# Kernel tuning notes

Measured on AMD Instinct MI355X. Metric: run time of the kernel, lower is better.

## Reference

```python
import jax, jax.numpy as jnp
import numpy as np

B, N, C = 2, 50000, 81          # images, proposals/image, classes (incl. background)
H, W = 800.0, 1333.0            # image shape
SCORE_THRESH = 0.05
NMS_THRESH = 0.5
DETS = 100                      # detections_per_img
K = 2048                        # pre-NMS candidates kept per image (padded)
BBOX_CLIP = 4.135166556742356   # log(1000/16), torchvision BoxCoder clamp
WX, WY, WW, WH = 10.0, 10.0, 5.0, 5.0  # bbox_reg_weights
MIN_SIZE = 0.01                 # remove_small_boxes threshold
LBL_OFFSET = 1401.0             # MAX_SIZE + 1, batched_nms class-offset trick


def setup_inputs() -> dict:
    key = jax.random.key(0)
    k1, k2, k3, k4 = jax.random.split(key, 4)
    class_logits = jax.random.normal(k1, (B * N, C), jnp.float32) * 2.0
    box_regression = jax.random.normal(k2, (B * N, C * 4), jnp.float32) * 0.5
    wh_img = jnp.array([W, H], jnp.float32)
    cxy = jax.random.uniform(k3, (B, N, 2), jnp.float32) * wh_img
    wh = jax.random.uniform(k4, (B, N, 2), jnp.float32) * 200.0 + 4.0
    x1y1 = jnp.clip(cxy - 0.5 * wh, 0.0, wh_img)
    x2y2 = jnp.clip(cxy + 0.5 * wh, 0.0, wh_img)
    proposals = jnp.concatenate([x1y1, x2y2], axis=-1)  # [B, N, 4] xyxy
    return {"class_logits": class_logits, "box_regression": box_regression, "proposals": proposals}


def _decode(rel, boxes):
    # rel [N, C, 4], boxes [N, 4] xyxy -> decoded [N, C, 4] (torchvision BoxCoder.decode)
    w = boxes[:, 2] - boxes[:, 0]
    h = boxes[:, 3] - boxes[:, 1]
    cx = boxes[:, 0] + 0.5 * w
    cy = boxes[:, 1] + 0.5 * h
    dx = rel[..., 0] / WX
    dy = rel[..., 1] / WY
    dw = jnp.minimum(rel[..., 2] / WW, BBOX_CLIP)
    dh = jnp.minimum(rel[..., 3] / WH, BBOX_CLIP)
    pcx = dx * w[:, None] + cx[:, None]
    pcy = dy * h[:, None] + cy[:, None]
    pw = jnp.exp(dw) * w[:, None]
    ph = jnp.exp(dh) * h[:, None]
    return jnp.stack([pcx - 0.5 * pw, pcy - 0.5 * ph, pcx + 0.5 * pw, pcy + 0.5 * ph], axis=-1)


def _pairwise_iou(a):
    # a [K, 4] -> [K, K]
    area = (a[:, 2] - a[:, 0]) * (a[:, 3] - a[:, 1])
    lt = jnp.maximum(a[:, None, :2], a[None, :, :2])
    rb = jnp.minimum(a[:, None, 2:], a[None, :, 2:])
    wh = jnp.clip(rb - lt, 0.0)
    inter = wh[..., 0] * wh[..., 1]
    return inter / (area[:, None] + area[None, :] - inter + 1e-9)


def _nms_keep(iou, valid):
    # sequential greedy NMS over score-sorted candidates
    Kn = iou.shape[0]
    def body(keep, i):
        sup = jnp.any(keep & (iou[i] > NMS_THRESH))
        keep = keep.at[i].set(valid[i] & ~sup)
        return keep, None
    keep, _ = jax.lax.scan(body, jnp.zeros((Kn,), bool), jnp.arange(Kn))
    return keep


def _per_image(logits, reg, props):
    # logits [N, C], reg [N, C*4], props [N, 4]
    scores = jax.nn.softmax(logits, axis=-1)[:, 1:]                  # drop background
    boxes = _decode(reg.reshape(N, C, 4), props)[:, 1:]              # [N, C-1, 4]
    boxes = jnp.stack([jnp.clip(boxes[..., 0], 0.0, W),
                       jnp.clip(boxes[..., 1], 0.0, H),
                       jnp.clip(boxes[..., 2], 0.0, W),
                       jnp.clip(boxes[..., 3], 0.0, H)], axis=-1)
    fb = boxes.reshape(-1, 4)                                        # [N*(C-1), 4]
    fs = scores.reshape(-1)
    fl = jnp.broadcast_to(jnp.arange(1, C), (N, C - 1)).reshape(-1)
    ws = fb[:, 2] - fb[:, 0]
    hs = fb[:, 3] - fb[:, 1]
    valid = (fs > SCORE_THRESH) & (ws >= MIN_SIZE) & (hs >= MIN_SIZE)
    masked = jnp.where(valid, fs, -1.0)
    top_s, top_i = jax.lax.top_k(masked, K)                          # sorted desc
    cb = fb[top_i]
    cl = fl[top_i]
    cvalid = top_s > 0.0
    # batched NMS: offset boxes by class so different classes never overlap
    ob = cb + cl.astype(cb.dtype)[:, None] * LBL_OFFSET
    keep = _nms_keep(_pairwise_iou(ob), cvalid)
    kept_s = jnp.where(keep, top_s, -1.0)
    out_s, sel = jax.lax.top_k(kept_s, DETS)
    m = out_s > 0.0
    out_b = cb[sel] * m[:, None].astype(cb.dtype)
    out_l = jnp.where(m, cl[sel], -1)
    return out_b, jnp.where(m, out_s, 0.0), out_l


def reference(class_logits, box_regression, proposals):
    logits = class_logits.reshape(B, N, C)
    reg = box_regression.reshape(B, N, C * 4)
    boxes, scores, labels = jax.vmap(_per_image)(logits, reg, proposals)
    return boxes, scores, labels  # [B, DETS, 4], [B, DETS], [B, DETS] (padded, score==0 invalid)
```

## Files before the change

kernel.cpp:

```cpp
#include <hip/hip_runtime.h>
#include <hip/hip_bf16.h>
#include <stdint.h>

#define Bn 2
#define Np 50000
#define Cc 81
#define CM1 80
#define KSEL 2048
#define NDET 100
#define NBUCK 2048
#define BUCK_BASE 0x3D000000u
#define BUCK_SHIFT 15
#define SELCAP 4096
#define IMG_W 1333.0f
#define IMG_H 800.0f
#define SCORE_TH 0.05f
#define MIN_SZ 0.01f
#define NMS_TH 0.5f
#define LBLOFF 1401.0f
#define BBOX_CLIP_F 4.135166556742356f
#define CHUNK 16
#define QCAP 320
#define BLKX 782
#define WPI  (BLKX*4)
#define RS_WPB 4

typedef unsigned long long u64;
typedef unsigned int u32;

__device__ __forceinline__ u64 shfl64(u64 v, int src) {
  int lo = __shfl((int)(u32)v, src, 64);
  int hi = __shfl((int)(u32)(v >> 32), src, 64);
  return ((u64)(u32)hi << 32) | (u32)lo;
}

__device__ __forceinline__ void decode_box(int row, int c,
    const float* __restrict__ reg, const float* __restrict__ props,
    float& x1, float& y1, float& x2, float& y2) {
  const float4 pr = *reinterpret_cast<const float4*>(props + (size_t)row * 4);
  float w = __fsub_rn(pr.z, pr.x), h = __fsub_rn(pr.w, pr.y);
  float cx = __fadd_rn(pr.x, 0.5f * w), cy = __fadd_rn(pr.y, 0.5f * h);
  const float4 rel = *reinterpret_cast<const float4*>(reg + ((size_t)row * Cc + c) * 4);
  float dx = __fdiv_rn(rel.x, 10.f), dy = __fdiv_rn(rel.y, 10.f);
  float dw = fminf(__fdiv_rn(rel.z, 5.f), BBOX_CLIP_F);
  float dh = fminf(__fdiv_rn(rel.w, 5.f), BBOX_CLIP_F);
  float pcx = __fadd_rn(__fmul_rn(dx, w), cx);
  float pcy = __fadd_rn(__fmul_rn(dy, h), cy);
  float pw = __fmul_rn(expf(dw), w);
  float ph = __fmul_rn(expf(dh), h);
  x1 = fminf(fmaxf(__fsub_rn(pcx, 0.5f * pw), 0.f), IMG_W);
  y1 = fminf(fmaxf(__fsub_rn(pcy, 0.5f * ph), 0.f), IMG_H);
  x2 = fminf(fmaxf(__fadd_rn(pcx, 0.5f * pw), 0.f), IMG_W);
  y2 = fminf(fmaxf(__fadd_rn(pcy, 0.5f * ph), 0.f), IMG_H);
}

#define SOFTMAX_PROLOG(S)                                            \
  const int p = lane >> 2, qd = lane & 3;                            \
  const int base = p * Cc + qd * 21;                                 \
  const int cnt_k = (qd == 3) ? 18 : 21;                             \
  float ev[21];                                                      \
  _Pragma("unroll")                                                  \
  for (int k = 0; k < 21; ++k)                                       \
    ev[k] = (k < cnt_k) ? (S)[base + k] : -3.4e38f;                  \
  float m = ev[0];                                                   \
  _Pragma("unroll")                                                  \
  for (int k = 1; k < 21; ++k) m = fmaxf(m, ev[k]);                  \
  m = fmaxf(m, __shfl_xor(m, 1, 64));                                \
  m = fmaxf(m, __shfl_xor(m, 2, 64));                                \
  float s = 0.f;                                                     \
  _Pragma("unroll")                                                  \
  for (int k = 0; k < 21; ++k) {                                     \
    ev[k] = (k < cnt_k) ? expf(ev[k] - m) : 0.f;                     \
    s += ev[k];                                                      \
  }                                                                  \
  s += __shfl_xor(s, 1, 64);                                         \
  s += __shfl_xor(s, 2, 64);                                         \
  const float thr = SCORE_TH * s;

#define STAGE_LOGITS(S, src)                                         \
  _Pragma("unroll")                                                  \
  for (int i = 0; i < 6; ++i) {                                      \
    const int f4 = i * 64 + lane;                                    \
    if (f4 < (CHUNK * Cc) / 4) {                                     \
      const float4 v = *reinterpret_cast<const float4*>((src) + (size_t)f4 * 4); \
      *reinterpret_cast<float4*>(&(S)[f4 * 4]) = v;                  \
    }                                                                \
  }

__global__ __launch_bounds__(256, 4) void passA_kernel(
    const float* __restrict__ logits, const float* __restrict__ reg,
    const float* __restrict__ props, u64* __restrict__ wseg,
    u32* __restrict__ wcnt, u32* __restrict__ ghist)
{
  __shared__ __align__(16) float stg[4][CHUNK * Cc];
  __shared__ u64 qbuf[4][QCAP];
  __shared__ u32 hist[NBUCK];
  const int b = blockIdx.y;
  const int tid = threadIdx.x;
  const int wave = tid >> 6, lane = tid & 63;
  for (int i = tid; i < NBUCK; i += 256) hist[i] = 0;
  __syncthreads();

  const int wslot = (blockIdx.x << 2) + wave;
  const int n0 = wslot * CHUNK;
  u64* Q = qbuf[wave];
  u32 qcnt = 0;
  if (n0 < Np) {
    float* S = stg[wave];
    STAGE_LOGITS(S, logits + ((size_t)b * Np + n0) * Cc)
    SOFTMAX_PROLOG(S)
    const int n_ = n0 + p;
    #pragma unroll
    for (int k = 0; k < 21; ++k) {
      const int c = qd * 21 + k;
      bool emit = false;
      u64 key = 0;
      if (c > 0 && ev[k] > thr) {
        const u32 sb = __float_as_uint(__fdiv_rn(ev[k], s));
        const u32 idx = (u32)(n_ * CM1 + (c - 1));
        key = ((u64)sb << 32) | (u32)(~idx);
        emit = true;
      }
      const u64 bal = __ballot(emit);
      if (emit) Q[qcnt + (u32)__popcll(bal & ((1ull << lane) - 1ull))] = key;
      qcnt += (u32)__popcll(bal);
    }
  }
  u64* seg = wseg + (size_t)(b * WPI + wslot) * QCAP;
  u32 wout = 0;
  for (u32 qb = 0; qb < qcnt; qb += 64) {
    const bool act = (qb + (u32)lane) < qcnt;
    u64 key = act ? Q[qb + lane] : 0ull;
    bool valid = false;
    u32 sb = 0;
    if (act) {
      sb = (u32)(key >> 32);
      const u32 idx = ~(u32)key;
      const int pn = (int)(idx / CM1);
      const int c = (int)(idx - (u32)pn * CM1) + 1;
      float x1, y1, x2, y2;
      decode_box(b * Np + pn, c, reg, props, x1, y1, x2, y2);
      valid = (__fsub_rn(x2, x1) >= MIN_SZ) && (__fsub_rn(y2, y1) >= MIN_SZ);
    }
    const u64 bal = __ballot(valid);
    if (valid) {
      const u32 pos = wout + (u32)__popcll(bal & ((1ull << lane) - 1ull));
      seg[pos] = key;
      u32 bk = (sb - BUCK_BASE) >> BUCK_SHIFT;
      if (bk > (u32)(NBUCK - 1)) bk = NBUCK - 1;
      atomicAdd(&hist[bk], 1u);
    }
    wout += (u32)__popcll(bal);
  }
  if (lane == 0) wcnt[b * WPI + wslot] = wout;
  __syncthreads();
  for (int i = tid; i < NBUCK; i += 256) {
    const u32 v = hist[i];
    if (v) atomicAdd(&ghist[b * NBUCK + i], v);
  }
}

__global__ void thresh_kernel(const u32* __restrict__ ghist, u32* __restrict__ gT,
                              u32* __restrict__ gTot, u32* __restrict__ boffs) {
  const int b = blockIdx.x;
  const int lane = threadIdx.x;
  const u32* h = ghist + b * NBUCK;
  u32* bo = boffs + b * NBUCK;
  const int SEG = NBUCK / 64;
  u32 segsum = 0;
  for (int t = 0; t < SEG; ++t) segsum += h[lane * SEG + t];
  u32 suf = segsum;
  #pragma unroll
  for (int o = 1; o < 64; o <<= 1) {
    const u32 v = (u32)__shfl_down((int)suf, o, 64);
    if (lane + o < 64) suf += v;
  }
  u32 acc = suf - segsum;
  int myT = -1; u32 totv = 0;
  for (int t = SEG - 1; t >= 0; --t) {
    const int bk = lane * SEG + t;
    bo[bk] = acc;
    acc += h[bk];
    if (myT < 0 && acc >= (u32)KSEL) { myT = bk; totv = acc; }
  }
  int Tg = myT;
  #pragma unroll
  for (int o = 32; o; o >>= 1) Tg = max(Tg, __shfl_xor(Tg, o, 64));
  if (Tg < 0) {
    if (lane == 0) { gT[b] = 0u; gTot[b] = (acc < (u32)SELCAP) ? acc : (u32)SELCAP; }
  } else if (myT == Tg) {
    gT[b] = (u32)Tg;
    gTot[b] = (totv < (u32)SELCAP) ? totv : (u32)SELCAP;
  }
}

__global__ __launch_bounds__(256) void scatter_kernel(
    const u64* __restrict__ wseg, const u32* __restrict__ wcnt,
    const u32* __restrict__ gT, const u32* __restrict__ boffs,
    u32* __restrict__ bfill, u64* __restrict__ skeys)
{
  const int b = blockIdx.y;
  const u32 T = gT[b];
  const int wave = threadIdx.x >> 6, lane = threadIdx.x & 63;
  const u32 sgi = blockIdx.x * 4 + wave;
  if (sgi >= (u32)WPI) return;
  const u32 cnt = wcnt[b * WPI + sgi];
  const u64* seg = wseg + (size_t)(b * WPI + sgi) * QCAP;
  for (u32 i = lane; i < cnt; i += 64) {
    const u64 key = seg[i];
    const u32 sb = (u32)(key >> 32);
    u32 bk = (sb - BUCK_BASE) >> BUCK_SHIFT;
    if (bk > (u32)(NBUCK - 1)) bk = NBUCK - 1;
    if (bk >= T) {
      const u32 pos = boffs[b * NBUCK + bk] + atomicAdd(&bfill[b * NBUCK + bk], 1u);
      if (pos < (u32)SELCAP) skeys[(size_t)b * SELCAP + pos] = key;
    }
  }
}

__global__ __launch_bounds__(256) void runsort_kernel(
    const u64* __restrict__ skeys, u64* __restrict__ skeys2,
    const u32* __restrict__ gT, const u32* __restrict__ gTot,
    const u32* __restrict__ boffs, const u32* __restrict__ bfill)
{
  const int b = blockIdx.y;
  const int wave = threadIdx.x >> 6, lane = threadIdx.x & 63;
  const u32 bk = blockIdx.x * RS_WPB + wave;
  if (bk >= (u32)NBUCK || bk < gT[b]) return;
  const u32 total = gTot[b];
  const u32 start = boffs[b * NBUCK + bk];
  u32 L = bfill[b * NBUCK + bk];
  if (L == 0 || start >= (u32)KSEL || start >= total) return;
  if (start + L > total) L = total - start;
  const u64* run = skeys + (size_t)b * SELCAP + start;
  u64* dst = skeys2 + (size_t)b * SELCAP + start;
  if (L <= 128u) {
    const u64 k0 = (lane < (int)L) ? run[lane] : 0ull;
    const u64 k1 = (64 + lane < (int)L) ? run[64 + lane] : 0ull;
    u32 r0 = 0, r1 = 0;
    #pragma unroll
    for (int l = 0; l < 64; ++l) {
      const u64 o0 = shfl64(k0, l);
      const u64 o1 = shfl64(k1, l);
      r0 += (o0 > k0) + (o1 > k0);
      r1 += (o0 > k1) + (o1 > k1);
    }
    if (lane < (int)L) dst[r0] = k0;
    if (64 + lane < (int)L) dst[r1] = k1;
  } else {
    for (u32 i = lane; i < L; i += 64) {
      const u64 k = run[i];
      u32 r = 0;
      for (u32 q = 0; q < L; ++q) r += (run[q] > k);
      dst[r] = k;
    }
  }
}

__global__ __launch_bounds__(1024) void tail_kernel(
    const u64* __restrict__ skeys2, const u32* __restrict__ gTot,
    const float* __restrict__ reg, const float* __restrict__ props,
    float* __restrict__ out)
{
  __shared__ u64 keys[KSEL];
  __shared__ float obx1[KSEL], oby1[KSEL], obx2[KSEL], oby2[KSEL];
  __shared__ float oar[KSEL], osc[KSEL];
  __shared__ unsigned short keptIdx[NDET];
  __shared__ u32 supflags[64];
  __shared__ u32 sh_kc;
  const int b = blockIdx.x;
  const int tid = threadIdx.x;
  const int wave = tid >> 6, lane = tid & 63;
  const u32 total = gTot[b];
  if (tid == 0) sh_kc = 0;

  for (int i = tid; i < KSEL; i += 1024)
    keys[i] = (i < (int)total) ? skeys2[(size_t)b * SELCAP + i] : 0ull;
  __syncthreads();

  for (int t = tid; t < KSEL; t += 1024) {
    const u64 key = keys[t];
    float x1 = 0, y1 = 0, x2 = 0, y2 = 0, score = 0, lab = 0;
    if (key) {
      const u32 sb = (u32)(key >> 32);
      const u32 idx = ~(u32)key;
      const int n_ = (int)(idx / CM1);
      const int c = (int)(idx % CM1) + 1;
      score = __uint_as_float(sb);
      decode_box(b * Np + n_, c, reg, props, x1, y1, x2, y2);
      lab = (float)c;
    }
    const float offv = __fmul_rn(lab, LBLOFF);
    const float ox1 = __fadd_rn(x1, offv), oy1 = __fadd_rn(y1, offv);
    const float ox2 = __fadd_rn(x2, offv), oy2 = __fadd_rn(y2, offv);
    obx1[t] = ox1; oby1[t] = oy1; obx2[t] = ox2; oby2[t] = oy2;
    oar[t] = __fmul_rn(__fsub_rn(ox2, ox1), __fsub_rn(oy2, oy1));
    osc[t] = score;
  }
  __syncthreads();

  int kc = 0;
  for (int c = 0; c < 32 && kc < NDET; ++c) {
    if (tid < 64) supflags[tid] = 0;
    __syncthreads();
    const int j = (c << 6) + lane;
    const float cx1 = obx1[j], cy1 = oby1[j], cx2 = obx2[j], cy2 = oby2[j], ca = oar[j];
    bool sup = false;
    for (int k = wave; k < kc; k += 16) {
      const int ki = keptIdx[k];
      const float ltx = fmaxf(cx1, obx1[ki]), lty = fmaxf(cy1, oby1[ki]);
      const float rbx = fminf(cx2, obx2[ki]), rby = fminf(cy2, oby2[ki]);
      const float wx = fmaxf(__fsub_rn(rbx, ltx), 0.f);
      const float wy = fmaxf(__fsub_rn(rby, lty), 0.f);
      const float inter = __fmul_rn(wx, wy);
      const float denom = __fadd_rn(__fsub_rn(__fadd_rn(ca, oar[ki]), inter), 1e-9f);
      if (__fdiv_rn(inter, denom) > NMS_TH) sup = true;
    }
    if (sup) supflags[lane] = 1u;
    __syncthreads();
    if (wave == 0) {
      u64 rem = __ballot(supflags[lane] != 0u);
      u64 todo = __ballot(osc[j] > 0.f) & ~rem;
      int kcl = kc;
      while (todo && kcl < NDET) {
        const int jb = (int)__builtin_ctzll(todo);
        const int cj = (c << 6) + jb;
        if (lane == 0) keptIdx[kcl] = (unsigned short)cj;
        ++kcl;
        const float kx1 = obx1[cj], ky1 = oby1[cj], kx2 = obx2[cj], ky2 = oby2[cj], ka = oar[cj];
        const float ltx = fmaxf(kx1, cx1), lty = fmaxf(ky1, cy1);
        const float rbx = fminf(kx2, cx2), rby = fminf(ky2, cy2);
        const float wx = fmaxf(__fsub_rn(rbx, ltx), 0.f);
        const float wy = fmaxf(__fsub_rn(rby, lty), 0.f);
        const float inter = __fmul_rn(wx, wy);
        const float denom = __fadd_rn(__fsub_rn(__fadd_rn(ka, ca), inter), 1e-9f);
        const u64 w = __ballot(__fdiv_rn(inter, denom) > NMS_TH);
        rem |= w;
        todo &= ~rem;
        todo &= ~(1ull << jb);
      }
      if (lane == 0) sh_kc = (u32)kcl;
    }
    __syncthreads();
    kc = (int)sh_kc;
  }

  __syncthreads();
  const int kcl = (kc < NDET) ? kc : NDET;
  if (tid < NDET) {
    float bx1 = 0, by1 = 0, bx2 = 0, by2 = 0, sc = 0, lb = -1.f;
    if (tid < kcl) {
      const int i = keptIdx[tid];
      const u64 key = keys[i];
      const u32 idx = ~(u32)key;
      const int n_ = (int)(idx / CM1);
      const int cc = (int)(idx % CM1) + 1;
      decode_box(b * Np + n_, cc, reg, props, bx1, by1, bx2, by2);
      sc = osc[i];
      lb = (float)cc;
    }
    float* ob = out + (size_t)b * NDET * 4;
    ob[tid * 4 + 0] = bx1; ob[tid * 4 + 1] = by1;
    ob[tid * 4 + 2] = bx2; ob[tid * 4 + 3] = by2;
    out[Bn * NDET * 4 + b * NDET + tid] = sc;
    out[Bn * NDET * 4 + Bn * NDET + b * NDET + tid] = lb;
  }
}

extern "C" void kernel_launch(void* const* d_in, const int* in_sizes, int n_in,
                              void* d_out, int out_size, void* d_ws, size_t ws_size,
                              hipStream_t stream) {
  const float* logits = (const float*)d_in[0];
  const float* reg    = (const float*)d_in[1];
  const float* props  = (const float*)d_in[2];
  float* out = (float*)d_out;
  char* ws = (char*)d_ws;

  u32* gT   = (u32*)ws;
  u32* gTot = (u32*)(ws + 16);
  size_t off = 64;
  u32* ghist  = (u32*)(ws + off); off += (size_t)Bn * NBUCK * 4;
  u32* bfill  = (u32*)(ws + off); off += (size_t)Bn * NBUCK * 4;
  const size_t memset_bytes = off;
  u32* boffs  = (u32*)(ws + off); off += (size_t)Bn * NBUCK * 4;
  u64* skeys  = (u64*)(ws + off); off += (size_t)Bn * SELCAP * 8;
  u64* skeys2 = (u64*)(ws + off); off += (size_t)Bn * SELCAP * 8;
  u32* wcnt   = (u32*)(ws + off); off += (size_t)Bn * WPI * 4;
  off = (off + 255) & ~(size_t)255;
  u64* wseg   = (u64*)(ws + off); off += (size_t)Bn * WPI * QCAP * 8;
  (void)ws_size;

  hipMemsetAsync(d_ws, 0, memset_bytes, stream);
  passA_kernel<<<dim3(BLKX, Bn), 256, 0, stream>>>(logits, reg, props, wseg, wcnt, ghist);
  thresh_kernel<<<dim3(Bn), 64, 0, stream>>>(ghist, gT, gTot, boffs);
  scatter_kernel<<<dim3((WPI + 3) / 4, Bn), 256, 0, stream>>>(wseg, wcnt, gT, boffs, bfill, skeys);
  runsort_kernel<<<dim3(NBUCK / RS_WPB, Bn), 256, 0, stream>>>(skeys, skeys2, gT, gTot, boffs, bfill);
  tail_kernel<<<dim3(Bn), 1024, 0, stream>>>(skeys2, gTot, reg, props, out);
}
```

Baseline: 85.50 us.

## Defer box decode and size filter to scatter; single-wave streaming NMS tail

Pass A no longer decodes boxes for every above-threshold candidate. The histogram now counts keys before the min-size filter, and the decode plus size check run only for keys in buckets at or above the threshold inside the scatter kernel. The run-sort kernel decodes the sorted keys into a structure-of-arrays selection buffer and zero-fills slots left by filtered boxes. The tail kernel becomes one 64-thread wave that walks the candidates in 64-wide chunks and exits early once 100 boxes are kept, instead of a 1024-thread block that decodes all 2048 candidates and synchronises each step. The risks are that the bucket threshold now counts invalid boxes, and that the serial tail may lengthen when many candidates are suppressed.

```diff
diff --git a/kernel.cpp b/kernel.cpp
--- a/kernel.cpp
+++ b/kernel.cpp
@@ -54,6 +54,21 @@
   y2 = fminf(fmaxf(__fadd_rn(pcy, 0.5f * ph), 0.f), IMG_H);
 }
 
+__device__ __forceinline__ void decode_key_to_sel(u64 key, int b,
+    const float* __restrict__ reg, const float* __restrict__ props,
+    float* __restrict__ S, u32 pos) {
+  const u32 sb = (u32)(key >> 32);
+  const u32 idx = ~(u32)key;
+  const int n_ = (int)(idx / CM1);
+  const int c = (int)(idx % CM1) + 1;
+  float x1, y1, x2, y2;
+  decode_box(b * Np + n_, c, reg, props, x1, y1, x2, y2);
+  S[0 * SELCAP + pos] = x1; S[1 * SELCAP + pos] = y1;
+  S[2 * SELCAP + pos] = x2; S[3 * SELCAP + pos] = y2;
+  S[4 * SELCAP + pos] = __uint_as_float(sb);
+  S[5 * SELCAP + pos] = (float)c;
+}
+
 #define SOFTMAX_PROLOG(S)                                            \
   const int p = lane >> 2, qd = lane & 3;                            \
   const int base = p * Cc + qd * 21;                                 \
@@ -88,12 +103,10 @@
   }
 
 __global__ __launch_bounds__(256, 4) void passA_kernel(
-    const float* __restrict__ logits, const float* __restrict__ reg,
-    const float* __restrict__ props, u64* __restrict__ wseg,
+    const float* __restrict__ logits, u64* __restrict__ wseg,
     u32* __restrict__ wcnt, u32* __restrict__ ghist)
 {
   __shared__ __align__(16) float stg[4][CHUNK * Cc];
-  __shared__ u64 qbuf[4][QCAP];
   __shared__ u32 hist[NBUCK];
   const int b = blockIdx.y;
   const int tid = threadIdx.x;
@@ -103,8 +116,8 @@
 
   const int wslot = (blockIdx.x << 2) + wave;
   const int n0 = wslot * CHUNK;
-  u64* Q = qbuf[wave];
-  u32 qcnt = 0;
+  u64* seg = wseg + (size_t)(b * WPI + wslot) * QCAP;
+  u32 wout = 0;
   if (n0 < Np) {
     float* S = stg[wave];
     STAGE_LOGITS(S, logits + ((size_t)b * Np + n0) * Cc)
@@ -114,43 +127,22 @@
     for (int k = 0; k < 21; ++k) {
       const int c = qd * 21 + k;
       bool emit = false;
-      u64 key = 0;
+      u64 key = 0; u32 bk = 0;
       if (c > 0 && ev[k] > thr) {
         const u32 sb = __float_as_uint(__fdiv_rn(ev[k], s));
         const u32 idx = (u32)(n_ * CM1 + (c - 1));
         key = ((u64)sb << 32) | (u32)(~idx);
+        bk = (sb - BUCK_BASE) >> BUCK_SHIFT;
+        if (bk > (u32)(NBUCK - 1)) bk = NBUCK - 1;
         emit = true;
       }
       const u64 bal = __ballot(emit);
-      if (emit) Q[qcnt + (u32)__popcll(bal & ((1ull << lane) - 1ull))] = key;
-      qcnt += (u32)__popcll(bal);
-    }
-  }
-  u64* seg = wseg + (size_t)(b * WPI + wslot) * QCAP;
-  u32 wout = 0;
-  for (u32 qb = 0; qb < qcnt; qb += 64) {
-    const bool act = (qb + (u32)lane) < qcnt;
-    u64 key = act ? Q[qb + lane] : 0ull;
-    bool valid = false;
-    u32 sb = 0;
-    if (act) {
-      sb = (u32)(key >> 32);
-      const u32 idx = ~(u32)key;
-      const int pn = (int)(idx / CM1);
-      const int c = (int)(idx - (u32)pn * CM1) + 1;
-      float x1, y1, x2, y2;
-      decode_box(b * Np + pn, c, reg, props, x1, y1, x2, y2);
-      valid = (__fsub_rn(x2, x1) >= MIN_SZ) && (__fsub_rn(y2, y1) >= MIN_SZ);
-    }
-    const u64 bal = __ballot(valid);
-    if (valid) {
-      const u32 pos = wout + (u32)__popcll(bal & ((1ull << lane) - 1ull));
-      seg[pos] = key;
-      u32 bk = (sb - BUCK_BASE) >> BUCK_SHIFT;
-      if (bk > (u32)(NBUCK - 1)) bk = NBUCK - 1;
-      atomicAdd(&hist[bk], 1u);
-    }
-    wout += (u32)__popcll(bal);
+      if (emit) {
+        seg[wout + (u32)__popcll(bal & ((1ull << lane) - 1ull))] = key;
+        atomicAdd(&hist[bk], 1u);
+      }
+      wout += (u32)__popcll(bal);
+    }
   }
   if (lane == 0) wcnt[b * WPI + wslot] = wout;
   __syncthreads();
@@ -197,7 +189,8 @@
 __global__ __launch_bounds__(256) void scatter_kernel(
     const u64* __restrict__ wseg, const u32* __restrict__ wcnt,
     const u32* __restrict__ gT, const u32* __restrict__ boffs,
-    u32* __restrict__ bfill, u64* __restrict__ skeys)
+    u32* __restrict__ bfill, u64* __restrict__ skeys,
+    const float* __restrict__ reg, const float* __restrict__ props)
 {
   const int b = blockIdx.y;
   const u32 T = gT[b];
@@ -212,31 +205,43 @@
     u32 bk = (sb - BUCK_BASE) >> BUCK_SHIFT;
     if (bk > (u32)(NBUCK - 1)) bk = NBUCK - 1;
     if (bk >= T) {
-      const u32 pos = boffs[b * NBUCK + bk] + atomicAdd(&bfill[b * NBUCK + bk], 1u);
-      if (pos < (u32)SELCAP) skeys[(size_t)b * SELCAP + pos] = key;
+      const u32 idx = ~(u32)key;
+      const int pn = (int)(idx / CM1);
+      const int c = (int)(idx % CM1) + 1;
+      float x1, y1, x2, y2;
+      decode_box(b * Np + pn, c, reg, props, x1, y1, x2, y2);
+      if (__fsub_rn(x2, x1) >= MIN_SZ && __fsub_rn(y2, y1) >= MIN_SZ) {
+        const u32 pos = boffs[b * NBUCK + bk] + atomicAdd(&bfill[b * NBUCK + bk], 1u);
+        if (pos < (u32)SELCAP) skeys[(size_t)b * SELCAP + pos] = key;
+      }
     }
   }
 }
 
 __global__ __launch_bounds__(256) void runsort_kernel(
-    const u64* __restrict__ skeys, u64* __restrict__ skeys2,
-    const u32* __restrict__ gT, const u32* __restrict__ gTot,
-    const u32* __restrict__ boffs, const u32* __restrict__ bfill)
+    const u64* __restrict__ skeys, const u32* __restrict__ gT,
+    const u32* __restrict__ boffs, const u32* __restrict__ bfill,
+    const u32* __restrict__ ghist,
+    const float* __restrict__ reg, const float* __restrict__ props,
+    float* __restrict__ sel)
 {
   const int b = blockIdx.y;
   const int wave = threadIdx.x >> 6, lane = threadIdx.x & 63;
   const u32 bk = blockIdx.x * RS_WPB + wave;
   if (bk >= (u32)NBUCK || bk < gT[b]) return;
-  const u32 total = gTot[b];
   const u32 start = boffs[b * NBUCK + bk];
-  u32 L = bfill[b * NBUCK + bk];
-  if (L == 0 || start >= (u32)KSEL || start >= total) return;
-  if (start + L > total) L = total - start;
+  if (start >= (u32)SELCAP) return;
+  u32 Lp = bfill[b * NBUCK + bk];
+  u32 Lh = ghist[b * NBUCK + bk];
+  if (start + Lp > (u32)SELCAP) Lp = SELCAP - start;
+  if (start + Lh > (u32)SELCAP) Lh = SELCAP - start;
+  float* S = sel + (size_t)b * 6 * SELCAP;
+  for (u32 j = Lp + lane; j < Lh; j += 64) S[4 * SELCAP + start + j] = 0.f;
+  if (Lp == 0) return;
   const u64* run = skeys + (size_t)b * SELCAP + start;
-  u64* dst = skeys2 + (size_t)b * SELCAP + start;
-  if (L <= 128u) {
-    const u64 k0 = (lane < (int)L) ? run[lane] : 0ull;
-    const u64 k1 = (64 + lane < (int)L) ? run[64 + lane] : 0ull;
+  if (Lp <= 128u) {
+    const u64 k0 = (lane < (int)Lp) ? run[lane] : 0ull;
+    const u64 k1 = (64 + lane < (int)Lp) ? run[64 + lane] : 0ull;
     u32 r0 = 0, r1 = 0;
     #pragma unroll
     for (int l = 0; l < 64; ++l) {
@@ -245,125 +250,89 @@
       r0 += (o0 > k0) + (o1 > k0);
       r1 += (o0 > k1) + (o1 > k1);
     }
-    if (lane < (int)L) dst[r0] = k0;
-    if (64 + lane < (int)L) dst[r1] = k1;
+    if (lane < (int)Lp) decode_key_to_sel(k0, b, reg, props, S, start + r0);
+    if (64 + lane < (int)Lp) decode_key_to_sel(k1, b, reg, props, S, start + r1);
   } else {
-    for (u32 i = lane; i < L; i += 64) {
+    for (u32 i = lane; i < Lp; i += 64) {
       const u64 k = run[i];
       u32 r = 0;
-      for (u32 q = 0; q < L; ++q) r += (run[q] > k);
-      dst[r] = k;
-    }
-  }
-}
-
-__global__ __launch_bounds__(1024) void tail_kernel(
-    const u64* __restrict__ skeys2, const u32* __restrict__ gTot,
-    const float* __restrict__ reg, const float* __restrict__ props,
+      for (u32 q = 0; q < Lp; ++q) r += (run[q] > k);
+      decode_key_to_sel(k, b, reg, props, S, start + r);
+    }
+  }
+}
+
+__global__ __launch_bounds__(64) void tail_kernel(
+    const float* __restrict__ sel, const u32* __restrict__ gTot,
     float* __restrict__ out)
 {
-  __shared__ u64 keys[KSEL];
-  __shared__ float obx1[KSEL], oby1[KSEL], obx2[KSEL], oby2[KSEL];
-  __shared__ float oar[KSEL], osc[KSEL];
-  __shared__ unsigned short keptIdx[NDET];
-  __shared__ u32 supflags[64];
-  __shared__ u32 sh_kc;
+  __shared__ float kox1[NDET], koy1[NDET], kox2[NDET], koy2[NDET], kar[NDET];
+  __shared__ float kx1[NDET], ky1[NDET], kx2[NDET], ky2[NDET], ksc[NDET], klb[NDET];
   const int b = blockIdx.x;
-  const int tid = threadIdx.x;
-  const int wave = tid >> 6, lane = tid & 63;
+  const int lane = threadIdx.x;
   const u32 total = gTot[b];
-  if (tid == 0) sh_kc = 0;
-
-  for (int i = tid; i < KSEL; i += 1024)
-    keys[i] = (i < (int)total) ? skeys2[(size_t)b * SELCAP + i] : 0ull;
-  __syncthreads();
-
-  for (int t = tid; t < KSEL; t += 1024) {
-    const u64 key = keys[t];
-    float x1 = 0, y1 = 0, x2 = 0, y2 = 0, score = 0, lab = 0;
-    if (key) {
-      const u32 sb = (u32)(key >> 32);
-      const u32 idx = ~(u32)key;
-      const int n_ = (int)(idx / CM1);
-      const int c = (int)(idx % CM1) + 1;
-      score = __uint_as_float(sb);
-      decode_box(b * Np + n_, c, reg, props, x1, y1, x2, y2);
-      lab = (float)c;
-    }
-    const float offv = __fmul_rn(lab, LBLOFF);
+  const float* S = sel + (size_t)b * 6 * SELCAP;
+  int kc = 0;
+  for (u32 bbase = 0; bbase < total && kc < NDET; bbase += 64) {
+    const u32 pos = bbase + lane;
+    const bool inb = pos < total;
+    float x1 = 0, y1 = 0, x2 = 0, y2 = 0, sc = 0, lb = 0;
+    if (inb) {
+      x1 = S[0 * SELCAP + pos]; y1 = S[1 * SELCAP + pos];
+      x2 = S[2 * SELCAP + pos]; y2 = S[3 * SELCAP + pos];
+      sc = S[4 * SELCAP + pos]; lb = S[5 * SELCAP + pos];
+    }
+    const float offv = __fmul_rn(lb, LBLOFF);
     const float ox1 = __fadd_rn(x1, offv), oy1 = __fadd_rn(y1, offv);
     const float ox2 = __fadd_rn(x2, offv), oy2 = __fadd_rn(y2, offv);
-    obx1[t] = ox1; oby1[t] = oy1; obx2[t] = ox2; oby2[t] = oy2;
-    oar[t] = __fmul_rn(__fsub_rn(ox2, ox1), __fsub_rn(oy2, oy1));
-    osc[t] = score;
-  }
-  __syncthreads();
-
-  int kc = 0;
-  for (int c = 0; c < 32 && kc < NDET; ++c) {
-    if (tid < 64) supflags[tid] = 0;
-    __syncthreads();
-    const int j = (c << 6) + lane;
-    const float cx1 = obx1[j], cy1 = oby1[j], cx2 = obx2[j], cy2 = oby2[j], ca = oar[j];
+    const float ar = __fmul_rn(__fsub_rn(ox2, ox1), __fsub_rn(oy2, oy1));
+    const bool valid = inb && (sc > 0.f);
     bool sup = false;
-    for (int k = wave; k < kc; k += 16) {
-      const int ki = keptIdx[k];
-      const float ltx = fmaxf(cx1, obx1[ki]), lty = fmaxf(cy1, oby1[ki]);
-      const float rbx = fminf(cx2, obx2[ki]), rby = fminf(cy2, oby2[ki]);
+    for (int k = 0; k < kc; ++k) {
+      const float ltx = fmaxf(ox1, kox1[k]), lty = fmaxf(oy1, koy1[k]);
+      const float rbx = fminf(ox2, kox2[k]), rby = fminf(oy2, koy2[k]);
       const float wx = fmaxf(__fsub_rn(rbx, ltx), 0.f);
       const float wy = fmaxf(__fsub_rn(rby, lty), 0.f);
       const float inter = __fmul_rn(wx, wy);
-      const float denom = __fadd_rn(__fsub_rn(__fadd_rn(ca, oar[ki]), inter), 1e-9f);
+      const float denom = __fadd_rn(__fsub_rn(__fadd_rn(ar, kar[k]), inter), 1e-9f);
       if (__fdiv_rn(inter, denom) > NMS_TH) sup = true;
     }
-    if (sup) supflags[lane] = 1u;
-    __syncthreads();
-    if (wave == 0) {
-      u64 rem = __ballot(supflags[lane] != 0u);
-      u64 todo = __ballot(osc[j] > 0.f) & ~rem;
-      int kcl = kc;
-      while (todo && kcl < NDET) {
-        const int jb = (int)__builtin_ctzll(todo);
-        const int cj = (c << 6) + jb;
-        if (lane == 0) keptIdx[kcl] = (unsigned short)cj;
-        ++kcl;
-        const float kx1 = obx1[cj], ky1 = oby1[cj], kx2 = obx2[cj], ky2 = oby2[cj], ka = oar[cj];
-        const float ltx = fmaxf(kx1, cx1), lty = fmaxf(ky1, cy1);
-        const float rbx = fminf(kx2, cx2), rby = fminf(ky2, cy2);
-        const float wx = fmaxf(__fsub_rn(rbx, ltx), 0.f);
-        const float wy = fmaxf(__fsub_rn(rby, lty), 0.f);
-        const float inter = __fmul_rn(wx, wy);
-        const float denom = __fadd_rn(__fsub_rn(__fadd_rn(ka, ca), inter), 1e-9f);
-        const u64 w = __ballot(__fdiv_rn(inter, denom) > NMS_TH);
-        rem |= w;
-        todo &= ~rem;
-        todo &= ~(1ull << jb);
+    u64 rem = __ballot(sup) | ~__ballot(valid);
+    u64 todo = ~rem;
+    while (todo && kc < NDET) {
+      const int jb = (int)__builtin_ctzll(todo);
+      const float bx1 = __shfl(ox1, jb, 64), by1 = __shfl(oy1, jb, 64);
+      const float bx2 = __shfl(ox2, jb, 64), by2 = __shfl(oy2, jb, 64);
+      const float ba  = __shfl(ar, jb, 64);
+      if (lane == jb) {
+        kox1[kc] = ox1; koy1[kc] = oy1; kox2[kc] = ox2; koy2[kc] = oy2; kar[kc] = ar;
+        kx1[kc] = x1; ky1[kc] = y1; kx2[kc] = x2; ky2[kc] = y2; ksc[kc] = sc; klb[kc] = lb;
       }
-      if (lane == 0) sh_kc = (u32)kcl;
-    }
-    __syncthreads();
-    kc = (int)sh_kc;
-  }
-
-  __syncthreads();
+      const float ltx = fmaxf(ox1, bx1), lty = fmaxf(oy1, by1);
+      const float rbx = fminf(ox2, bx2), rby = fminf(oy2, by2);
+      const float wx = fmaxf(__fsub_rn(rbx, ltx), 0.f);
+      const float wy = fmaxf(__fsub_rn(rby, lty), 0.f);
+      const float inter = __fmul_rn(wx, wy);
+      const float denom = __fadd_rn(__fsub_rn(__fadd_rn(ar, ba), inter), 1e-9f);
+      const u64 w = __ballot(__fdiv_rn(inter, denom) > NMS_TH);
+      rem |= w;
+      todo &= ~rem;
+      todo &= ~(1ull << jb);
+      ++kc;
+    }
+  }
   const int kcl = (kc < NDET) ? kc : NDET;
-  if (tid < NDET) {
+  for (int k = lane; k < NDET; k += 64) {
     float bx1 = 0, by1 = 0, bx2 = 0, by2 = 0, sc = 0, lb = -1.f;
-    if (tid < kcl) {
-      const int i = keptIdx[tid];
-      const u64 key = keys[i];
-      const u32 idx = ~(u32)key;
-      const int n_ = (int)(idx / CM1);
-      const int cc = (int)(idx % CM1) + 1;
-      decode_box(b * Np + n_, cc, reg, props, bx1, by1, bx2, by2);
-      sc = osc[i];
-      lb = (float)cc;
+    if (k < kcl) {
+      bx1 = kx1[k]; by1 = ky1[k]; bx2 = kx2[k]; by2 = ky2[k];
+      sc = ksc[k]; lb = klb[k];
     }
     float* ob = out + (size_t)b * NDET * 4;
-    ob[tid * 4 + 0] = bx1; ob[tid * 4 + 1] = by1;
-    ob[tid * 4 + 2] = bx2; ob[tid * 4 + 3] = by2;
-    out[Bn * NDET * 4 + b * NDET + tid] = sc;
-    out[Bn * NDET * 4 + Bn * NDET + b * NDET + tid] = lb;
+    ob[k * 4 + 0] = bx1; ob[k * 4 + 1] = by1;
+    ob[k * 4 + 2] = bx2; ob[k * 4 + 3] = by2;
+    out[Bn * NDET * 4 + b * NDET + k] = sc;
+    out[Bn * NDET * 4 + Bn * NDET + b * NDET + k] = lb;
   }
 }
 
@@ -379,21 +348,21 @@
   u32* gT   = (u32*)ws;
   u32* gTot = (u32*)(ws + 16);
   size_t off = 64;
-  u32* ghist  = (u32*)(ws + off); off += (size_t)Bn * NBUCK * 4;
-  u32* bfill  = (u32*)(ws + off); off += (size_t)Bn * NBUCK * 4;
+  u32* ghist = (u32*)(ws + off); off += (size_t)Bn * NBUCK * 4;
+  u32* bfill = (u32*)(ws + off); off += (size_t)Bn * NBUCK * 4;
   const size_t memset_bytes = off;
-  u32* boffs  = (u32*)(ws + off); off += (size_t)Bn * NBUCK * 4;
-  u64* skeys  = (u64*)(ws + off); off += (size_t)Bn * SELCAP * 8;
-  u64* skeys2 = (u64*)(ws + off); off += (size_t)Bn * SELCAP * 8;
-  u32* wcnt   = (u32*)(ws + off); off += (size_t)Bn * WPI * 4;
+  u32* boffs = (u32*)(ws + off); off += (size_t)Bn * NBUCK * 4;
+  u64* skeys = (u64*)(ws + off); off += (size_t)Bn * SELCAP * 8;
+  float* sel = (float*)(ws + off); off += (size_t)Bn * 6 * SELCAP * 4;
+  u32* wcnt  = (u32*)(ws + off); off += (size_t)Bn * WPI * 4;
   off = (off + 255) & ~(size_t)255;
-  u64* wseg   = (u64*)(ws + off); off += (size_t)Bn * WPI * QCAP * 8;
+  u64* wseg  = (u64*)(ws + off); off += (size_t)Bn * WPI * QCAP * 8;
   (void)ws_size;
 
   hipMemsetAsync(d_ws, 0, memset_bytes, stream);
-  passA_kernel<<<dim3(BLKX, Bn), 256, 0, stream>>>(logits, reg, props, wseg, wcnt, ghist);
+  passA_kernel<<<dim3(BLKX, Bn), 256, 0, stream>>>(logits, wseg, wcnt, ghist);
   thresh_kernel<<<dim3(Bn), 64, 0, stream>>>(ghist, gT, gTot, boffs);
-  scatter_kernel<<<dim3((WPI + 3) / 4, Bn), 256, 0, stream>>>(wseg, wcnt, gT, boffs, bfill, skeys);
-  runsort_kernel<<<dim3(NBUCK / RS_WPB, Bn), 256, 0, stream>>>(skeys, skeys2, gT, gTot, boffs, bfill);
-  tail_kernel<<<dim3(Bn), 1024, 0, stream>>>(skeys2, gTot, reg, props, out);
-}
+  scatter_kernel<<<dim3((WPI + 3) / 4, Bn), 256, 0, stream>>>(wseg, wcnt, gT, boffs, bfill, skeys, reg, props);
+  runsort_kernel<<<dim3(NBUCK / RS_WPB, Bn), 256, 0, stream>>>(skeys, gT, boffs, bfill, ghist, reg, props, sel);
+  tail_kernel<<<dim3(Bn), 64, 0, stream>>>(sel, gTot, out);
+}
```

New measurement: 89.98 us. 5.2% more time.

## Drop LDS logit staging, process two row chunks per wave, prefix-scan compaction

Applied to the files above, without the earlier changes.

passA now reads each lane's 21 logits straight from global memory instead of staging through shared memory. Each wave handles 32 proposals in two rounds, so half as many blocks are launched. Candidate compaction moves from one ballot per class to a per-lane emit mask plus a wave prefix scan, and the drain loop is factored into a helper. The bfill zeroing moves from the memset into thresh_kernel, shrinking the memset, at the cost of uncoalesced strided global loads and less parallelism.

```diff
diff --git a/kernel.cpp b/kernel.cpp
--- a/kernel.cpp
+++ b/kernel.cpp
@@ -19,9 +19,9 @@
 #define NMS_TH 0.5f
 #define LBLOFF 1401.0f
 #define BBOX_CLIP_F 4.135166556742356f
-#define CHUNK 16
+#define CHUNK 32
 #define QCAP 320
-#define BLKX 782
+#define BLKX 391
 #define WPI  (BLKX*4)
 #define RS_WPB 4
 
@@ -54,83 +54,12 @@
   y2 = fminf(fmaxf(__fadd_rn(pcy, 0.5f * ph), 0.f), IMG_H);
 }
 
-#define SOFTMAX_PROLOG(S)                                            \
-  const int p = lane >> 2, qd = lane & 3;                            \
-  const int base = p * Cc + qd * 21;                                 \
-  const int cnt_k = (qd == 3) ? 18 : 21;                             \
-  float ev[21];                                                      \
-  _Pragma("unroll")                                                  \
-  for (int k = 0; k < 21; ++k)                                       \
-    ev[k] = (k < cnt_k) ? (S)[base + k] : -3.4e38f;                  \
-  float m = ev[0];                                                   \
-  _Pragma("unroll")                                                  \
-  for (int k = 1; k < 21; ++k) m = fmaxf(m, ev[k]);                  \
-  m = fmaxf(m, __shfl_xor(m, 1, 64));                                \
-  m = fmaxf(m, __shfl_xor(m, 2, 64));                                \
-  float s = 0.f;                                                     \
-  _Pragma("unroll")                                                  \
-  for (int k = 0; k < 21; ++k) {                                     \
-    ev[k] = (k < cnt_k) ? expf(ev[k] - m) : 0.f;                     \
-    s += ev[k];                                                      \
-  }                                                                  \
-  s += __shfl_xor(s, 1, 64);                                         \
-  s += __shfl_xor(s, 2, 64);                                         \
-  const float thr = SCORE_TH * s;
-
-#define STAGE_LOGITS(S, src)                                         \
-  _Pragma("unroll")                                                  \
-  for (int i = 0; i < 6; ++i) {                                      \
-    const int f4 = i * 64 + lane;                                    \
-    if (f4 < (CHUNK * Cc) / 4) {                                     \
-      const float4 v = *reinterpret_cast<const float4*>((src) + (size_t)f4 * 4); \
-      *reinterpret_cast<float4*>(&(S)[f4 * 4]) = v;                  \
-    }                                                                \
-  }
-
-__global__ __launch_bounds__(256, 4) void passA_kernel(
-    const float* __restrict__ logits, const float* __restrict__ reg,
-    const float* __restrict__ props, u64* __restrict__ wseg,
-    u32* __restrict__ wcnt, u32* __restrict__ ghist)
-{
-  __shared__ __align__(16) float stg[4][CHUNK * Cc];
-  __shared__ u64 qbuf[4][QCAP];
-  __shared__ u32 hist[NBUCK];
-  const int b = blockIdx.y;
-  const int tid = threadIdx.x;
-  const int wave = tid >> 6, lane = tid & 63;
-  for (int i = tid; i < NBUCK; i += 256) hist[i] = 0;
-  __syncthreads();
-
-  const int wslot = (blockIdx.x << 2) + wave;
-  const int n0 = wslot * CHUNK;
-  u64* Q = qbuf[wave];
-  u32 qcnt = 0;
-  if (n0 < Np) {
-    float* S = stg[wave];
-    STAGE_LOGITS(S, logits + ((size_t)b * Np + n0) * Cc)
-    SOFTMAX_PROLOG(S)
-    const int n_ = n0 + p;
-    #pragma unroll
-    for (int k = 0; k < 21; ++k) {
-      const int c = qd * 21 + k;
-      bool emit = false;
-      u64 key = 0;
-      if (c > 0 && ev[k] > thr) {
-        const u32 sb = __float_as_uint(__fdiv_rn(ev[k], s));
-        const u32 idx = (u32)(n_ * CM1 + (c - 1));
-        key = ((u64)sb << 32) | (u32)(~idx);
-        emit = true;
-      }
-      const u64 bal = __ballot(emit);
-      if (emit) Q[qcnt + (u32)__popcll(bal & ((1ull << lane) - 1ull))] = key;
-      qcnt += (u32)__popcll(bal);
-    }
-  }
-  u64* seg = wseg + (size_t)(b * WPI + wslot) * QCAP;
-  u32 wout = 0;
-  for (u32 qb = 0; qb < qcnt; qb += 64) {
-    const bool act = (qb + (u32)lane) < qcnt;
-    u64 key = act ? Q[qb + lane] : 0ull;
+__device__ __forceinline__ u32 drain(const u64* Qb, u32 n, int lane, int b,
+    const float* __restrict__ reg, const float* __restrict__ props,
+    u32* hist, u64* seg, u32 wout) {
+  for (u32 qb = 0; qb < n; qb += 64) {
+    const bool act = (qb + (u32)lane) < n;
+    u64 key = act ? Qb[qb + lane] : 0ull;
     bool valid = false;
     u32 sb = 0;
     if (act) {
@@ -144,13 +73,84 @@
     }
     const u64 bal = __ballot(valid);
     if (valid) {
-      const u32 pos = wout + (u32)__popcll(bal & ((1ull << lane) - 1ull));
-      seg[pos] = key;
+      seg[wout + (u32)__popcll(bal & ((1ull << lane) - 1ull))] = key;
       u32 bk = (sb - BUCK_BASE) >> BUCK_SHIFT;
       if (bk > (u32)(NBUCK - 1)) bk = NBUCK - 1;
       atomicAdd(&hist[bk], 1u);
     }
     wout += (u32)__popcll(bal);
+  }
+  return wout;
+}
+
+__global__ __launch_bounds__(256, 4) void passA_kernel(
+    const float* __restrict__ logits, const float* __restrict__ reg,
+    const float* __restrict__ props, u64* __restrict__ wseg,
+    u32* __restrict__ wcnt, u32* __restrict__ ghist)
+{
+  __shared__ u64 qbuf[4][QCAP];
+  __shared__ u32 hist[NBUCK];
+  const int b = blockIdx.y;
+  const int tid = threadIdx.x;
+  const int wave = tid >> 6, lane = tid & 63;
+  for (int i = tid; i < NBUCK; i += 256) hist[i] = 0;
+  __syncthreads();
+
+  const int wslot = (blockIdx.x << 2) + wave;
+  u64* Q = qbuf[wave];
+  u64* seg = wseg + (size_t)(b * WPI + wslot) * QCAP;
+  u32 wout = 0;
+  const int p = lane >> 2, qd = lane & 3;
+  const int cnt_k = (qd == 3) ? 18 : 21;
+  #pragma unroll
+  for (int r = 0; r < 2; ++r) {
+    const int n0 = wslot * CHUNK + r * 16;
+    if (n0 >= Np) break;
+    const int n_ = n0 + p;
+    const float* lrow = logits + ((size_t)b * Np + n_) * Cc + qd * 21;
+    float ev[21];
+    #pragma unroll
+    for (int k = 0; k < 21; ++k)
+      ev[k] = (k < cnt_k) ? lrow[k] : -3.4e38f;
+    float m = ev[0];
+    #pragma unroll
+    for (int k = 1; k < 21; ++k) m = fmaxf(m, ev[k]);
+    m = fmaxf(m, __shfl_xor(m, 1, 64));
+    m = fmaxf(m, __shfl_xor(m, 2, 64));
+    float s = 0.f;
+    #pragma unroll
+    for (int k = 0; k < 21; ++k) {
+      ev[k] = (k < cnt_k) ? expf(ev[k] - m) : 0.f;
+      s += ev[k];
+    }
+    s += __shfl_xor(s, 1, 64);
+    s += __shfl_xor(s, 2, 64);
+    const float thr = SCORE_TH * s;
+    u32 emask = 0;
+    #pragma unroll
+    for (int k = 0; k < 21; ++k) {
+      const int c = qd * 21 + k;
+      if (c > 0 && ev[k] > thr) emask |= (1u << k);
+    }
+    const u32 mycnt = __popc(emask);
+    u32 inc = mycnt;
+    #pragma unroll
+    for (int o = 1; o < 64; o <<= 1) {
+      const u32 v = (u32)__shfl_up((int)inc, o, 64);
+      if (lane >= o) inc += v;
+    }
+    u32 pos = inc - mycnt;
+    const u32 qtot = (u32)__shfl((int)inc, 63, 64);
+    u32 em = emask;
+    while (em) {
+      const int k = (int)__builtin_ctz(em);
+      em &= em - 1;
+      const int c = qd * 21 + k;
+      const u32 sb = __float_as_uint(__fdiv_rn(ev[k], s));
+      const u32 idx = (u32)(n_ * CM1 + (c - 1));
+      Q[pos++] = ((u64)sb << 32) | (u32)(~idx);
+    }
+    wout = drain(Q, qtot, lane, b, reg, props, hist, seg, wout);
   }
   if (lane == 0) wcnt[b * WPI + wslot] = wout;
   __syncthreads();
@@ -161,7 +161,8 @@
 }
 
 __global__ void thresh_kernel(const u32* __restrict__ ghist, u32* __restrict__ gT,
-                              u32* __restrict__ gTot, u32* __restrict__ boffs) {
+                              u32* __restrict__ gTot, u32* __restrict__ boffs,
+                              u32* __restrict__ bfill) {
   const int b = blockIdx.x;
   const int lane = threadIdx.x;
   const u32* h = ghist + b * NBUCK;
@@ -180,6 +181,7 @@
   for (int t = SEG - 1; t >= 0; --t) {
     const int bk = lane * SEG + t;
     bo[bk] = acc;
+    bfill[b * NBUCK + bk] = 0u;
     acc += h[bk];
     if (myT < 0 && acc >= (u32)KSEL) { myT = bk; totv = acc; }
   }
@@ -380,8 +382,8 @@
   u32* gTot = (u32*)(ws + 16);
   size_t off = 64;
   u32* ghist  = (u32*)(ws + off); off += (size_t)Bn * NBUCK * 4;
+  const size_t memset_bytes = off;
   u32* bfill  = (u32*)(ws + off); off += (size_t)Bn * NBUCK * 4;
-  const size_t memset_bytes = off;
   u32* boffs  = (u32*)(ws + off); off += (size_t)Bn * NBUCK * 4;
   u64* skeys  = (u64*)(ws + off); off += (size_t)Bn * SELCAP * 8;
   u64* skeys2 = (u64*)(ws + off); off += (size_t)Bn * SELCAP * 8;
@@ -392,7 +394,7 @@
 
   hipMemsetAsync(d_ws, 0, memset_bytes, stream);
   passA_kernel<<<dim3(BLKX, Bn), 256, 0, stream>>>(logits, reg, props, wseg, wcnt, ghist);
-  thresh_kernel<<<dim3(Bn), 64, 0, stream>>>(ghist, gT, gTot, boffs);
+  thresh_kernel<<<dim3(Bn), 64, 0, stream>>>(ghist, gT, gTot, boffs, bfill);
   scatter_kernel<<<dim3((WPI + 3) / 4, Bn), 256, 0, stream>>>(wseg, wcnt, gT, boffs, bfill, skeys);
   runsort_kernel<<<dim3(NBUCK / RS_WPB, Bn), 256, 0, stream>>>(skeys, skeys2, gT, gTot, boffs, bfill);
   tail_kernel<<<dim3(Bn), 1024, 0, stream>>>(skeys2, gTot, reg, props, out);
```

New measurement: 78.13 us. -8.6%, faster.
